# Kernel optimization log

Hardware: AMD Instinct MI355X
Metric: run time of the kernel (lower is better)

Reference implementation:

```python
import jax, jax.numpy as jnp
import numpy as np

B, L, F = 4096, 128, 64
NODE_MAX = 1024  # padding id is 0


def setup_inputs() -> dict:
    key = jax.random.key(0)
    k1, k2, k3, k4, k5, k6 = jax.random.split(key, 6)
    src_ids = jax.random.randint(k1, (B, L), 0, NODE_MAX, dtype=jnp.int64)
    dst_ids = jax.random.randint(k2, (B, L), 0, NODE_MAX, dtype=jnp.int64)
    W1 = jax.random.normal(k3, (1, F), dtype=jnp.float32)
    b1 = jax.random.normal(k4, (F,), dtype=jnp.float32)
    W2 = jax.random.normal(k5, (F, F), dtype=jnp.float32) / jnp.sqrt(F)
    b2 = jax.random.normal(k6, (F,), dtype=jnp.float32)
    return {"src_ids": src_ids, "dst_ids": dst_ids, "W1": W1, "b1": b1, "W2": W2, "b2": b2}


def _pair_counts(a, b):
    """For each element of a[bi, i]: (count of that id in a's row, count in b's row).

    Equality-based counting is exactly equivalent to np.unique counts + dict lookup
    (missing ids simply match nothing -> count 0).
    """
    self_cnt = (a[:, :, None] == a[:, None, :]).astype(jnp.float32).sum(-1)   # [B,L]
    cross_cnt = (a[:, :, None] == b[:, None, :]).astype(jnp.float32).sum(-1)  # [B,L]
    return self_cnt, cross_cnt


def _encode(freq, W1, b1, W2, b2):
    # freq: [B,L,2] -> unsqueeze to [B,L,2,1] -> MLP -> sum over the 2-axis -> [B,L,F]
    h = jax.nn.relu(freq[..., None] * W1[0] + b1)          # [B,L,2,F]
    out = jnp.einsum("blcf,fg->blcg", h, W2) + b2          # [B,L,2,F]
    return out.sum(axis=2)                                  # [B,L,F]


def reference(src_ids, dst_ids, W1, b1, W2, b2):
    src_self, src_cross = _pair_counts(src_ids, dst_ids)
    dst_self, dst_cross = _pair_counts(dst_ids, src_ids)
    src_mask = (src_ids != 0).astype(jnp.float32)[..., None]  # zero padded positions
    dst_mask = (dst_ids != 0).astype(jnp.float32)[..., None]
    # source rows: [freq in src, freq in dst]; dst rows: [freq in dst, freq in src]
    src_freq = jnp.stack([src_self, src_cross], axis=-1) * src_mask  # [B,L,2]
    dst_freq = jnp.stack([dst_self, dst_cross], axis=-1) * dst_mask  # [B,L,2]
    src_feat = _encode(src_freq, W1, b1, W2, b2)
    dst_feat = _encode(dst_freq, W1, b1, W2, b2)
    return src_feat, dst_feat
```

## Files before the change

### kernel.cpp

```cpp
#include <hip/hip_runtime.h>

#define BDIM 4096
#define LDIM 128
#define FDIM 64
#define NVALS 129
#define NODE_MAX 1024

typedef float f32x4 __attribute__((ext_vector_type(4)));

__global__ __launch_bounds__(FDIM) void build_table_kernel(
    const float* __restrict__ W1, const float* __restrict__ b1,
    const float* __restrict__ W2, const float* __restrict__ b2,
    float* __restrict__ T)
{
    const int v = blockIdx.x;
    const int g = threadIdx.x;

    __shared__ float h[FDIM];
    h[g] = fmaxf((float)v * W1[g] + b1[g], 0.0f);
    __syncthreads();

    float acc = b2[g];
#pragma unroll
    for (int f = 0; f < FDIM; ++f)
        acc = fmaf(h[f], W2[f * FDIM + g], acc);

    T[v * FDIM + g] = acc;
}

__global__ __launch_bounds__(256) void encode_rows_kernel(
    const int* __restrict__ src, const int* __restrict__ dst,
    const float* __restrict__ T,
    float* __restrict__ out_src, float* __restrict__ out_dst)
{
    const int b = blockIdx.x;
    const int t = threadIdx.x;

    __shared__ int sID[LDIM], dID[LDIM];
    __shared__ int histS[NODE_MAX], histD[NODE_MAX];
    __shared__ int aS[LDIM], bS[LDIM], aD[LDIM], bD[LDIM];

    ((int4*)histS)[t] = make_int4(0, 0, 0, 0);
    ((int4*)histD)[t] = make_int4(0, 0, 0, 0);
    if (t < LDIM) sID[t] = src[(size_t)b * LDIM + t];
    else          dID[t - LDIM] = dst[(size_t)b * LDIM + (t - LDIM)];
    __syncthreads();

    if (t < LDIM) atomicAdd(&histS[sID[t]], 1);
    else          atomicAdd(&histD[dID[t - LDIM]], 1);
    __syncthreads();

    if (t < LDIM) {
        const int id = sID[t];
        int a = histS[id], c = histD[id];
        if (id == 0) { a = 0; c = 0; }
        aS[t] = a; bS[t] = c;
    } else {
        const int id = dID[t - LDIM];
        int a = histD[id], c = histS[id];
        if (id == 0) { a = 0; c = 0; }
        aD[t - LDIM] = a; bD[t - LDIM] = c;
    }
    __syncthreads();

    const f32x4* __restrict__ T4 = (const f32x4*)T;
    f32x4* __restrict__ o4s = (f32x4*)out_src;
    f32x4* __restrict__ o4d = (f32x4*)out_dst;
    const size_t rowBase = (size_t)b * (LDIM * FDIM / 4);

#pragma unroll
    for (int k = 0; k < 8; ++k) {
        const int c   = t + k * 256;
        const int pos = c >> 4;
        const int ch  = c & 15;

        {
            const f32x4 r = T4[aS[pos] * 16 + ch] + T4[bS[pos] * 16 + ch];
            __builtin_nontemporal_store(r, &o4s[rowBase + c]);
        }
        {
            const f32x4 r = T4[aD[pos] * 16 + ch] + T4[bD[pos] * 16 + ch];
            __builtin_nontemporal_store(r, &o4d[rowBase + c]);
        }
    }
}

extern "C" void kernel_launch(void* const* d_in, const int* in_sizes, int n_in,
                              void* d_out, int out_size, void* d_ws, size_t ws_size,
                              hipStream_t stream)
{
    const int*   src = (const int*)d_in[0];
    const int*   dst = (const int*)d_in[1];
    const float* W1  = (const float*)d_in[2];
    const float* b1  = (const float*)d_in[3];
    const float* W2  = (const float*)d_in[4];
    const float* b2  = (const float*)d_in[5];

    float* out = (float*)d_out;
    float* T   = (float*)d_ws;

    const int B = in_sizes[0] / LDIM;
    const size_t half = (size_t)B * LDIM * FDIM;

    build_table_kernel<<<NVALS, FDIM, 0, stream>>>(W1, b1, W2, b2, T);
    encode_rows_kernel<<<B, 256, 0, stream>>>(src, dst, T, out, out + half);
}
```

Measured before the change: 60.02 us.

## Split histogram prep from output streaming and merge table build into prep

Merges the lookup-table build into a new prep kernel, which also computes the per-position count pairs for every row and packs each pair into a 16-bit index stored in workspace. A separate grid-stride streaming kernel then gathers two table rows per element and writes the full output with ordinary stores in place of nontemporal ones. The goal is to decouple the latency-bound histogram phase from the bandwidth-bound write phase so each runs at full occupancy. In exchange it adds an extra global round trip for the index array, and it needs enough workspace, otherwise it falls back to the old fused kernel.

```diff
diff --git a/kernel.cpp b/kernel.cpp
--- a/kernel.cpp
+++ b/kernel.cpp
@@ -1,6 +1,5 @@
 #include <hip/hip_runtime.h>
 
-#define BDIM 4096
 #define LDIM 128
 #define FDIM 64
 #define NVALS 129
@@ -8,24 +7,72 @@
 
 typedef float f32x4 __attribute__((ext_vector_type(4)));
 
-__global__ __launch_bounds__(FDIM) void build_table_kernel(
+__global__ __launch_bounds__(256) void prep_kernel(
+    const int* __restrict__ src, const int* __restrict__ dst,
     const float* __restrict__ W1, const float* __restrict__ b1,
     const float* __restrict__ W2, const float* __restrict__ b2,
-    float* __restrict__ T)
+    float* __restrict__ T, unsigned short* __restrict__ idx, int B)
 {
-    const int v = blockIdx.x;
-    const int g = threadIdx.x;
+    const int t = threadIdx.x;
 
-    __shared__ float h[FDIM];
-    h[g] = fmaxf((float)v * W1[g] + b1[g], 0.0f);
+    if (blockIdx.x < 33) {
+        const int vi = t >> 6, g = t & 63;
+        const int v  = blockIdx.x * 4 + vi;
+        __shared__ float h[4][FDIM];
+        h[vi][g] = fmaxf((float)v * W1[g] + b1[g], 0.0f);
+        __syncthreads();
+        if (v < NVALS) {
+            float acc = b2[g];
+#pragma unroll
+            for (int f = 0; f < FDIM; ++f)
+                acc = fmaf(h[vi][f], W2[f * FDIM + g], acc);
+            T[v * FDIM + g] = acc;
+        }
+        return;
+    }
+
+    const int row = blockIdx.x - 33;
+    __shared__ int sID[LDIM], dID[LDIM];
+    __shared__ int histS[NODE_MAX], histD[NODE_MAX];
+
+    ((int4*)histS)[t] = make_int4(0, 0, 0, 0);
+    ((int4*)histD)[t] = make_int4(0, 0, 0, 0);
+    if (t < LDIM) sID[t] = src[(size_t)row * LDIM + t];
+    else          dID[t - LDIM] = dst[(size_t)row * LDIM + (t - LDIM)];
     __syncthreads();
 
-    float acc = b2[g];
-#pragma unroll
-    for (int f = 0; f < FDIM; ++f)
-        acc = fmaf(h[f], W2[f * FDIM + g], acc);
+    if (t < LDIM) atomicAdd(&histS[sID[t]], 1);
+    else          atomicAdd(&histD[dID[t - LDIM]], 1);
+    __syncthreads();
 
-    T[v * FDIM + g] = acc;
+    if (t < LDIM) {
+        const int id = sID[t];
+        int a = histS[id], c = histD[id];
+        if (id == 0) { a = 0; c = 0; }
+        idx[(size_t)row * LDIM + t] = (unsigned short)(a | (c << 8));
+    } else {
+        const int p = t - LDIM;
+        const int id = dID[p];
+        int a = histD[id], c = histS[id];
+        if (id == 0) { a = 0; c = 0; }
+        idx[(size_t)(B + row) * LDIM + p] = (unsigned short)(a | (c << 8));
+    }
+}
+
+__global__ __launch_bounds__(256) void stream_kernel(
+    const unsigned short* __restrict__ idx, const float* __restrict__ T,
+    f32x4* __restrict__ out, int total4)
+{
+    const f32x4* __restrict__ T4 = (const f32x4*)T;
+    const int tid    = blockIdx.x * 256 + threadIdx.x;
+    const int stride = gridDim.x * 256;
+#pragma unroll 8
+    for (int c = tid; c < total4; c += stride) {
+        const int e  = c >> 4;
+        const int ch = c & 15;
+        const unsigned int p = idx[e];
+        out[c] = T4[(p & 255u) * 16 + ch] + T4[(p >> 8) * 16 + ch];
+    }
 }
 
 __global__ __launch_bounds__(256) void encode_rows_kernel(
@@ -73,15 +120,8 @@
         const int c   = t + k * 256;
         const int pos = c >> 4;
         const int ch  = c & 15;
-
-        {
-            const f32x4 r = T4[aS[pos] * 16 + ch] + T4[bS[pos] * 16 + ch];
-            __builtin_nontemporal_store(r, &o4s[rowBase + c]);
-        }
-        {
-            const f32x4 r = T4[aD[pos] * 16 + ch] + T4[bD[pos] * 16 + ch];
-            __builtin_nontemporal_store(r, &o4d[rowBase + c]);
-        }
+        o4s[rowBase + c] = T4[aS[pos] * 16 + ch] + T4[bS[pos] * 16 + ch];
+        o4d[rowBase + c] = T4[aD[pos] * 16 + ch] + T4[bD[pos] * 16 + ch];
     }
 }
 
@@ -100,8 +140,19 @@
     float* T   = (float*)d_ws;
 
     const int B = in_sizes[0] / LDIM;
-    const size_t half = (size_t)B * LDIM * FDIM;
+    const size_t idx_off   = 33280;
+    const size_t idx_bytes = (size_t)2 * B * LDIM * sizeof(unsigned short);
 
-    build_table_kernel<<<NVALS, FDIM, 0, stream>>>(W1, b1, W2, b2, T);
-    encode_rows_kernel<<<B, 256, 0, stream>>>(src, dst, T, out, out + half);
+    if (ws_size >= idx_off + idx_bytes) {
+        unsigned short* idx = (unsigned short*)((char*)d_ws + idx_off);
+        const int total4 = 2 * B * LDIM * (FDIM / 4);
+        const int nblk   = (total4 / (256 * 8)) > 0 ? (total4 / (256 * 8)) : 1;
+        prep_kernel<<<33 + B, 256, 0, stream>>>(src, dst, W1, b1, W2, b2, T, idx, B);
+        stream_kernel<<<nblk, 256, 0, stream>>>(idx, T, (f32x4*)out, total4);
+    } else {
+        prep_kernel<<<33, 256, 0, stream>>>(src, dst, W1, b1, W2, b2, T,
+                                            (unsigned short*)nullptr, B);
+        const size_t half = (size_t)B * LDIM * FDIM;
+        encode_rows_kernel<<<B, 256, 0, stream>>>(src, dst, T, out, out + half);
+    }
 }
```

Measured after the change: 53.37 us. 1.12x faster.
